# Kernel optimization log

Hardware: AMD Instinct MI355X
Metric: run time of the kernel (lower is better)

## Reference

```python
import jax, jax.numpy as jnp
import numpy as np

B, Q, H, NH, HD = 2, 1024, 2048, 16, 128
QKV_ALPHA = 1e-4   # W8A8B8O8Linear output scale (a)
QKV_BETA = 1.0     # W8A8B8O8Linear bias scale (b)
QK_SCALE = 1e-4    # BMM_S8T_S8N_F32T dequant scale
PV_SCALE = 2e-3    # BMM_S8T_S8N_S8T output scale
DENSE_ALPHA = 1e-5 # W8A8BFP32OFP32Linear dequant scale
INV_NORM = 1.0 / (HD ** 0.5)


def setup_inputs() -> dict:
    key = jax.random.key(0)
    ks = jax.random.split(key, 8)
    hidden_states = jax.random.randint(ks[0], (B, Q, H), -128, 128, dtype=jnp.int32)  # int8 activations
    residual = jax.random.normal(ks[1], (B, Q, H), dtype=jnp.float32)
    alibi = jax.random.normal(ks[2], (B * NH, 1, Q), dtype=jnp.float32) * 0.1
    causal = jnp.triu(jnp.ones((Q, Q), dtype=bool), k=1)  # True = masked (future positions)
    attention_mask = jnp.broadcast_to(causal[None, None], (B, 1, Q, Q))
    w_qkv = jax.random.randint(ks[3], (3 * H, H), -128, 128, dtype=jnp.int32)   # int8 weight
    b_qkv = jax.random.randint(ks[4], (3 * H,), -128, 128, dtype=jnp.int32)     # int8 bias
    w_dense = jax.random.randint(ks[5], (H, H), -128, 128, dtype=jnp.int32)     # int8 weight
    b_dense = jax.random.normal(ks[6], (H,), dtype=jnp.float32)                 # fp32 bias
    return dict(hidden_states=hidden_states, residual=residual, alibi=alibi,
                attention_mask=attention_mask, w_qkv=w_qkv, b_qkv=b_qkv,
                w_dense=w_dense, b_dense=b_dense)


def _quant_i8(x_f32):
    return jnp.clip(jnp.round(x_f32), -128, 127).astype(jnp.int32)


def reference(hidden_states, residual, alibi, attention_mask, w_qkv, b_qkv, w_dense, b_dense):
    # --- W8A8B8O8 fused QKV linear: int8 in, int8 out ---
    acc = jnp.einsum('bqh,oh->bqo', hidden_states, w_qkv)  # exact int32 accumulation
    fused_qkv = _quant_i8(acc.astype(jnp.float32) * QKV_ALPHA + b_qkv.astype(jnp.float32) * QKV_BETA)
    # _split_heads: [B,Q,3H] -> [B,Q,NH,3,HD]
    qkv = fused_qkv.reshape(B, Q, NH, 3, HD)
    q = qkv[..., 0, :].transpose(0, 2, 1, 3).reshape(B * NH, Q, HD)
    k = qkv[..., 1, :].transpose(0, 2, 1, 3).reshape(B * NH, Q, HD)
    v = qkv[..., 2, :].transpose(0, 2, 1, 3).reshape(B * NH, Q, HD)
    # --- BMM_S8T_S8N_F32T: int8 q @ k^T -> fp32 * scale, plus alibi bias ---
    scores_i32 = jnp.einsum('nqd,nkd->nqk', q, k)  # [B*NH,Q,KV] int32
    matmul_result = alibi * 1.0 + scores_i32.astype(jnp.float32) * QK_SCALE * INV_NORM
    attention_scores = matmul_result.reshape(B, NH, Q, Q)
    # masked softmax (True = masked)
    attn_weights = jnp.where(attention_mask, jnp.finfo(jnp.float32).min, attention_scores)
    attention_probs = jax.nn.softmax(attn_weights, axis=-1)
    # quantize probs to int8 with scale 1/127 (BMM_S8T_S8N_S8T A-side)
    p_i8 = _quant_i8(attention_probs * 127.0).reshape(B * NH, Q, Q)
    # --- BMM_S8T_S8N_S8T: int8 probs @ int8 v -> int8 context ---
    ctx_acc = jnp.einsum('nqk,nkd->nqd', p_i8, v)  # int32
    ctx_i8 = _quant_i8(ctx_acc.astype(jnp.float32) * PV_SCALE)
    # _merge_heads: [B*NH,Q,HD] -> [B,Q,H]
    ctx = ctx_i8.reshape(B, NH, Q, HD).transpose(0, 2, 1, 3).reshape(B, Q, H)
    # --- W8A8BFP32OFP32 dense: int8 in, fp32 out ---
    dense_acc = jnp.einsum('bqh,oh->bqo', ctx, w_dense)
    output = dense_acc.astype(jnp.float32) * DENSE_ALPHA + b_dense + residual
    return output
```

## Files before the change

kernel.cpp:

```cpp
#include <hip/hip_runtime.h>
#include <stdint.h>

typedef int i32x4 __attribute__((ext_vector_type(4)));

#define DEV __device__ __forceinline__

DEV void glds16(const void* g, void* l) {
  __builtin_amdgcn_global_load_lds(
      (const __attribute__((address_space(1))) void*)g,
      (__attribute__((address_space(3))) void*)l, 16, 0, 0);
}

DEV int clampi8(float f) {
  int v = (int)rintf(f);
  return v < -128 ? -128 : (v > 127 ? 127 : v);
}

__global__ void pack_all_kernel(const int* __restrict__ s0, const int* __restrict__ s1,
                                const int* __restrict__ s2, int8_t* __restrict__ d0,
                                int8_t* __restrict__ d1, int8_t* __restrict__ d2) {
  const int i = blockIdx.x * 256 + threadIdx.x;
  const int* s;
  int8_t* d;
  int j;
  if (i < 1048576) { s = s0; d = d0; j = i; }
  else if (i < 4194304) { s = s1; d = d1; j = i - 1048576; }
  else { s = s2; d = d2; j = i - 4194304; }
  int4 v = ((const int4*)s)[j];
  char4 c;
  c.x = (char)v.x; c.y = (char)v.y; c.z = (char)v.z; c.w = (char)v.w;
  ((char4*)d)[j] = c;
}

template<int K>
DEV void gemm_core(const int8_t* __restrict__ A, const int8_t* __restrict__ B,
                   int row0, int col0, i32x4 acc[4][4], char* lA, char* lB,
                   int l, int w, int wm, int wn) {
  const int lr = l & 15, lg = l >> 4;
  const int8_t* pA0 = A + (size_t)(row0 + (w * 2 + 0) * 16 + lr) * K + lg * 16;
  const int8_t* pA1 = A + (size_t)(row0 + (w * 2 + 1) * 16 + lr) * K + lg * 16;
  const int8_t* pB0 = B + (size_t)(col0 + (w * 2 + 0) * 16 + lr) * K + lg * 16;
  const int8_t* pB1 = B + (size_t)(col0 + (w * 2 + 1) * 16 + lr) * K + lg * 16;
  glds16(pA0, lA + (w * 2 + 0) * 1024);
  glds16(pA1, lA + (w * 2 + 1) * 1024);
  glds16(pB0, lB + (w * 2 + 0) * 1024);
  glds16(pB1, lB + (w * 2 + 1) * 1024);
  __syncthreads();
  int cur = 0;
  for (int k0 = 0; k0 < K; k0 += 64) {
    const int nxt = cur ^ 1;
    if (k0 + 64 < K) {
      glds16(pA0 + k0 + 64, lA + nxt * 8192 + (w * 2 + 0) * 1024);
      glds16(pA1 + k0 + 64, lA + nxt * 8192 + (w * 2 + 1) * 1024);
      glds16(pB0 + k0 + 64, lB + nxt * 8192 + (w * 2 + 0) * 1024);
      glds16(pB1 + k0 + 64, lB + nxt * 8192 + (w * 2 + 1) * 1024);
    }
    i32x4 a[4], b[4];
#pragma unroll
    for (int i = 0; i < 4; ++i)
      a[i] = *(const i32x4*)(lA + cur * 8192 + ((wm * 4 + i) * 64 + l) * 16);
#pragma unroll
    for (int j = 0; j < 4; ++j)
      b[j] = *(const i32x4*)(lB + cur * 8192 + ((wn * 4 + j) * 64 + l) * 16);
#pragma unroll
    for (int i = 0; i < 4; ++i)
#pragma unroll
      for (int j = 0; j < 4; ++j)
        acc[i][j] = __builtin_amdgcn_mfma_i32_16x16x64_i8(a[i], b[j], acc[i][j], 0, 0, 0);
    __syncthreads();
    cur = nxt;
  }
}

__global__ __launch_bounds__(256) void qkv_kernel(
    const int8_t* __restrict__ hs8, const int8_t* __restrict__ w8,
    const int* __restrict__ bq, int8_t* __restrict__ qb, int8_t* __restrict__ kb,
    int8_t* __restrict__ vT) {
  __shared__ __align__(16) char lA[16384];
  __shared__ __align__(16) char lB[16384];
  const int l = threadIdx.x & 63, w = threadIdx.x >> 6;
  const int wm = w >> 1, wn = w & 1;
  const int lr = l & 15, lg = l >> 4;
  const int row0 = blockIdx.y * 128, col0 = blockIdx.x * 128;
  i32x4 acc[4][4] = {};
  gemm_core<2048>(hs8, w8, row0, col0, acc, lA, lB, l, w, wm, wn);
#pragma unroll
  for (int j = 0; j < 4; ++j) {
    const int col = col0 + (wn * 4 + j) * 16 + lr;
    const float bias = (float)bq[col];
    const int nh = col / 384, rem = col - nh * 384;
    const int s = rem >> 7, d = rem & 127;
#pragma unroll
    for (int i = 0; i < 4; ++i) {
#pragma unroll
      for (int r = 0; r < 4; ++r) {
        const int row = row0 + (wm * 4 + i) * 16 + lg * 4 + r;
        const int bb = row >> 10, qpos = row & 1023;
        const int n = bb * 16 + nh;
        const int8_t c = (int8_t)clampi8((float)acc[i][j][r] * 1e-4f + bias);
        if (s == 0)      qb[((size_t)n << 17) + (qpos << 7) + d] = c;
        else if (s == 1) kb[((size_t)n << 17) + (qpos << 7) + d] = c;
        else             vT[((size_t)n << 17) + (d << 10) + qpos] = c;
      }
    }
  }
}

__global__ __launch_bounds__(256) void attn_stats_kernel(
    const int8_t* __restrict__ qb, const int8_t* __restrict__ kb,
    const float* __restrict__ alibi, float* __restrict__ stats) {
  const int n = blockIdx.y;
  const int tri = blockIdx.x;
  int qt = 0;
  while ((qt + 1) * (qt + 2) / 2 <= tri) ++qt;
  const int kt = tri - qt * (qt + 1) / 2;
  const int l = threadIdx.x & 63, w = threadIdx.x >> 6;
  const int lr = l & 15, lg = l >> 4;
  const int row0 = qt * 128;
  const int8_t* Qh = qb + ((size_t)n << 17);
  const int8_t* Kh = kb + ((size_t)n << 17);
  const float* al = alibi + n * 1024;

  i32x4 qa[2][2];
#pragma unroll
  for (int t = 0; t < 2; ++t)
#pragma unroll
    for (int ks = 0; ks < 2; ++ks)
      qa[t][ks] = *(const i32x4*)(Qh + (size_t)(row0 + (w * 2 + t) * 16 + lr) * 128 + ks * 64 + lg * 16);

  float sf[2][8][4];
#pragma unroll
  for (int nf = 0; nf < 8; ++nf) {
    const size_t krow = (size_t)(kt * 128 + nf * 16 + lr) * 128;
    const i32x4 bk0 = *(const i32x4*)(Kh + krow + lg * 16);
    const i32x4 bk1 = *(const i32x4*)(Kh + krow + 64 + lg * 16);
    const int col = kt * 128 + nf * 16 + lr;
    const float av = al[col];
#pragma unroll
    for (int t = 0; t < 2; ++t) {
      i32x4 sa = {0, 0, 0, 0};
      sa = __builtin_amdgcn_mfma_i32_16x16x64_i8(qa[t][0], bk0, sa, 0, 0, 0);
      sa = __builtin_amdgcn_mfma_i32_16x16x64_i8(qa[t][1], bk1, sa, 0, 0, 0);
#pragma unroll
      for (int r = 0; r < 4; ++r) {
        const int rowg = row0 + (w * 2 + t) * 16 + lg * 4 + r;
        sf[t][nf][r] = (col <= rowg)
            ? av + ((float)sa[r] * 1e-4f) * 0.08838834764831843f
            : -INFINITY;
      }
    }
  }
#pragma unroll
  for (int t = 0; t < 2; ++t)
#pragma unroll
    for (int r = 0; r < 4; ++r) {
      float tm = sf[t][0][r];
#pragma unroll
      for (int nf = 1; nf < 8; ++nf) tm = fmaxf(tm, sf[t][nf][r]);
#pragma unroll
      for (int o = 1; o < 16; o <<= 1) tm = fmaxf(tm, __shfl_xor(tm, o));
      float es = 0.f;
#pragma unroll
      for (int nf = 0; nf < 8; ++nf) es += __expf(sf[t][nf][r] - tm);
#pragma unroll
      for (int o = 1; o < 16; o <<= 1) es += __shfl_xor(es, o);
      if (lr == 0) {
        const int rowl = (w * 2 + t) * 16 + lg * 4 + r;
        float2* st = (float2*)stats;
        st[((n * 8 + qt) * 8 + kt) * 128 + rowl] = make_float2(tm, es);
      }
    }
}

__global__ __launch_bounds__(256) void attn_pv_kernel(
    const int8_t* __restrict__ qb, const int8_t* __restrict__ kb,
    const int8_t* __restrict__ vT, const float* __restrict__ alibi,
    const float* __restrict__ stats, int* __restrict__ slab0,
    int* __restrict__ slab1, int8_t* __restrict__ ctx) {
  __shared__ __align__(16) char lP[128 * 144];
  const int n = blockIdx.y, gi = blockIdx.x;
  int qt, g, kt0, kt1;
  if (gi < 4) { qt = gi; g = 0; kt0 = 0; kt1 = qt + 1; }
  else { const int p = gi - 4; qt = 4 + (p >> 1); g = p & 1; kt0 = g ? 4 : 0; kt1 = g ? qt + 1 : 4; }
  const int l = threadIdx.x & 63, w = threadIdx.x >> 6;
  const int lr = l & 15, lg = l >> 4;
  const int row0 = qt * 128;
  const int8_t* Qh = qb + ((size_t)n << 17);
  const int8_t* Kh = kb + ((size_t)n << 17);
  const int8_t* Vh = vT + ((size_t)n << 17);
  const float* al = alibi + n * 1024;

  i32x4 qa[2][2];
#pragma unroll
  for (int t = 0; t < 2; ++t)
#pragma unroll
    for (int ks = 0; ks < 2; ++ks)
      qa[t][ks] = *(const i32x4*)(Qh + (size_t)(row0 + (w * 2 + t) * 16 + lr) * 128 + ks * 64 + lg * 16);

  float mrow[2][4], srow[2][4];
  const float2* st = (const float2*)stats;
#pragma unroll
  for (int t = 0; t < 2; ++t)
#pragma unroll
    for (int r = 0; r < 4; ++r) {
      const int rowl = (w * 2 + t) * 16 + lg * 4 + r;
      const int base = ((n * 8 + qt) * 8) * 128 + rowl;
      float m = -INFINITY;
      for (int k2 = 0; k2 <= qt; ++k2) m = fmaxf(m, st[base + k2 * 128].x);
      float s = 0.f;
      for (int k2 = 0; k2 <= qt; ++k2) {
        const float2 p = st[base + k2 * 128];
        s += p.y * __expf(p.x - m);
      }
      mrow[t][r] = m; srow[t][r] = s;
    }

  i32x4 pacc[2][8] = {};
  for (int kt = kt0; kt < kt1; ++kt) {
#pragma unroll
    for (int nf = 0; nf < 8; ++nf) {
      const size_t krow = (size_t)(kt * 128 + nf * 16 + lr) * 128;
      const i32x4 bk0 = *(const i32x4*)(Kh + krow + lg * 16);
      const i32x4 bk1 = *(const i32x4*)(Kh + krow + 64 + lg * 16);
      const int col = kt * 128 + nf * 16 + lr;
      const float av = al[col];
#pragma unroll
      for (int t = 0; t < 2; ++t) {
        i32x4 sa = {0, 0, 0, 0};
        sa = __builtin_amdgcn_mfma_i32_16x16x64_i8(qa[t][0], bk0, sa, 0, 0, 0);
        sa = __builtin_amdgcn_mfma_i32_16x16x64_i8(qa[t][1], bk1, sa, 0, 0, 0);
#pragma unroll
        for (int r = 0; r < 4; ++r) {
          const int rowl = (w * 2 + t) * 16 + lg * 4 + r;
          const int rowg = row0 + rowl;
          int p = 0;
          if (col <= rowg) {
            const float s = av + ((float)sa[r] * 1e-4f) * 0.08838834764831843f;
            p = (int)rintf(__expf(s - mrow[t][r]) / srow[t][r] * 127.0f);
          }
          lP[rowl * 144 + nf * 16 + lr] = (char)p;
        }
      }
    }
    __syncthreads();
#pragma unroll
    for (int t = 0; t < 2; ++t) {
      const int rowl = (w * 2 + t) * 16 + lr;
      const i32x4 pa0 = *(const i32x4*)(lP + rowl * 144 + lg * 16);
      const i32x4 pa1 = *(const i32x4*)(lP + rowl * 144 + 64 + lg * 16);
#pragma unroll
      for (int nf = 0; nf < 8; ++nf) {
        const size_t vrow = (size_t)(nf * 16 + lr) * 1024 + kt * 128;
        const i32x4 vb0 = *(const i32x4*)(Vh + vrow + lg * 16);
        const i32x4 vb1 = *(const i32x4*)(Vh + vrow + 64 + lg * 16);
        pacc[t][nf] = __builtin_amdgcn_mfma_i32_16x16x64_i8(pa0, vb0, pacc[t][nf], 0, 0, 0);
        pacc[t][nf] = __builtin_amdgcn_mfma_i32_16x16x64_i8(pa1, vb1, pacc[t][nf], 0, 0, 0);
      }
    }
  }
  const int bb = n >> 4, nh = n & 15;
  if (qt < 4) {
#pragma unroll
    for (int t = 0; t < 2; ++t)
#pragma unroll
      for (int nf = 0; nf < 8; ++nf)
#pragma unroll
        for (int r = 0; r < 4; ++r) {
          const int qpos = row0 + (w * 2 + t) * 16 + lg * 4 + r;
          const int d = nf * 16 + lr;
          ctx[((size_t)(bb * 1024 + qpos)) * 2048 + nh * 128 + d] =
              (int8_t)clampi8((float)pacc[t][nf][r] * 2e-3f);
        }
  } else {
    int* slab = g ? slab1 : slab0;
#pragma unroll
    for (int t = 0; t < 2; ++t)
#pragma unroll
      for (int nf = 0; nf < 8; ++nf)
#pragma unroll
        for (int r = 0; r < 4; ++r) {
          const int qpos = row0 + (w * 2 + t) * 16 + lg * 4 + r;
          const int d = nf * 16 + lr;
          slab[(size_t)(bb * 512 + qpos - 512) * 2048 + nh * 128 + d] = pacc[t][nf][r];
        }
  }
}

__global__ void ctx_reduce_kernel(const int* __restrict__ slab0,
                                  const int* __restrict__ slab1,
                                  int8_t* __restrict__ ctx) {
  const int i = blockIdx.x * blockDim.x + threadIdx.x;
  const int4 a = ((const int4*)slab0)[i];
  const int4 b = ((const int4*)slab1)[i];
  const int elem0 = i * 4;
  const int r512 = elem0 >> 11, col = elem0 & 2047;
  const int bb = r512 >> 9, qpos = 512 + (r512 & 511);
  char4 c;
  c.x = (char)clampi8((float)(a.x + b.x) * 2e-3f);
  c.y = (char)clampi8((float)(a.y + b.y) * 2e-3f);
  c.z = (char)clampi8((float)(a.z + b.z) * 2e-3f);
  c.w = (char)clampi8((float)(a.w + b.w) * 2e-3f);
  ((char4*)ctx)[((size_t)(bb * 1024 + qpos) * 2048 + col) >> 2] = c;
}

__global__ __launch_bounds__(256) void dense_kernel(
    const int8_t* __restrict__ c8, const int8_t* __restrict__ w8,
    const float* __restrict__ bd, const float* __restrict__ res,
    float* __restrict__ out) {
  __shared__ __align__(16) char lA[16384];
  __shared__ __align__(16) char lB[8192];
  const int l = threadIdx.x & 63, w = threadIdx.x >> 6;
  const int wm = w >> 1, wn = w & 1;
  const int lr = l & 15, lg = l >> 4;
  const int row0 = blockIdx.y * 128, col0 = blockIdx.x * 64;
  const int8_t* pA0 = c8 + (size_t)(row0 + (w * 2 + 0) * 16 + lr) * 2048 + lg * 16;
  const int8_t* pA1 = c8 + (size_t)(row0 + (w * 2 + 1) * 16 + lr) * 2048 + lg * 16;
  const int8_t* pB  = w8 + (size_t)(col0 + w * 16 + lr) * 2048 + lg * 16;
  glds16(pA0, lA + (w * 2 + 0) * 1024);
  glds16(pA1, lA + (w * 2 + 1) * 1024);
  glds16(pB,  lB + w * 1024);
  __syncthreads();
  i32x4 acc[4][2] = {};
  int cur = 0;
  for (int k0 = 0; k0 < 2048; k0 += 64) {
    const int nxt = cur ^ 1;
    if (k0 + 64 < 2048) {
      glds16(pA0 + k0 + 64, lA + nxt * 8192 + (w * 2 + 0) * 1024);
      glds16(pA1 + k0 + 64, lA + nxt * 8192 + (w * 2 + 1) * 1024);
      glds16(pB + k0 + 64, lB + nxt * 4096 + w * 1024);
    }
    i32x4 a[4], b[2];
#pragma unroll
    for (int i = 0; i < 4; ++i)
      a[i] = *(const i32x4*)(lA + cur * 8192 + ((wm * 4 + i) * 64 + l) * 16);
#pragma unroll
    for (int j = 0; j < 2; ++j)
      b[j] = *(const i32x4*)(lB + cur * 4096 + ((wn * 2 + j) * 64 + l) * 16);
#pragma unroll
    for (int i = 0; i < 4; ++i)
#pragma unroll
      for (int j = 0; j < 2; ++j)
        acc[i][j] = __builtin_amdgcn_mfma_i32_16x16x64_i8(a[i], b[j], acc[i][j], 0, 0, 0);
    __syncthreads();
    cur = nxt;
  }
#pragma unroll
  for (int j = 0; j < 2; ++j) {
    const int col = col0 + (wn * 2 + j) * 16 + lr;
    const float bias = bd[col];
#pragma unroll
    for (int i = 0; i < 4; ++i) {
#pragma unroll
      for (int r = 0; r < 4; ++r) {
        const int row = row0 + (wm * 4 + i) * 16 + lg * 4 + r;
        const size_t o = (size_t)row * 2048 + col;
        out[o] = (float)acc[i][j][r] * 1e-5f + bias + res[o];
      }
    }
  }
}

extern "C" void kernel_launch(void* const* d_in, const int* in_sizes, int n_in,
                              void* d_out, int out_size, void* d_ws, size_t ws_size,
                              hipStream_t stream) {
  const int* hs = (const int*)d_in[0];
  const float* res = (const float*)d_in[1];
  const float* alibi = (const float*)d_in[2];
  const int* wqkv = (const int*)d_in[4];
  const int* bqkv = (const int*)d_in[5];
  const int* wd = (const int*)d_in[6];
  const float* bd = (const float*)d_in[7];
  float* out = (float*)d_out;
  char* ws = (char*)d_ws;

  int8_t* hs8   = (int8_t*)(ws + 0);
  int8_t* wqkv8 = (int8_t*)(ws + 4194304);
  int*    slab0 = (int*)(ws + 0);
  int*    slab1 = (int*)(ws + 8388608);
  int8_t* wd8   = (int8_t*)(ws + 16777216);
  int8_t* q8b   = (int8_t*)(ws + 20971520);
  int8_t* k8b   = (int8_t*)(ws + 25165824);
  int8_t* vT8   = (int8_t*)(ws + 29360128);
  int8_t* ctx8  = (int8_t*)(ws + 33554432);
  float*  stats = (float*)(ws + 37748736);

  pack_all_kernel<<<20480, 256, 0, stream>>>(hs, wqkv, wd, hs8, wqkv8, wd8);
  qkv_kernel<<<dim3(48, 16), 256, 0, stream>>>(hs8, wqkv8, bqkv, q8b, k8b, vT8);
  attn_stats_kernel<<<dim3(36, 32), 256, 0, stream>>>(q8b, k8b, alibi, stats);
  attn_pv_kernel<<<dim3(12, 32), 256, 0, stream>>>(q8b, k8b, vT8, alibi, stats,
                                                   slab0, slab1, ctx8);
  ctx_reduce_kernel<<<2048, 256, 0, stream>>>(slab0, slab1, ctx8);
  dense_kernel<<<dim3(32, 16), 256, 0, stream>>>(ctx8, wd8, bd, res, out);
}
```

Measured before the change: 197.6 us.

## Split attention PV into two-tile KV chunks with atomic int32 accumulation

The PV kernel now splits every query tile into chunks of at most two KV tiles, which raises the grid from 12 to 20 blocks per head. Partial int32 context sums are combined with atomicAdd into a zeroed full-size accumulator, and a separate kernel then quantizes that accumulator to int8. This replaces the two-slab split plus reduce kernel and aims for better load balance across the causal triangle. In exchange it adds a 16MB zeroing pass, atomic write traffic for every query tile, and a full-size quantize read. A __syncthreads between writing P to LDS and reading it back is also removed, which holds only because each wave reads back just its own rows.

```diff
diff --git a/kernel.cpp b/kernel.cpp
--- a/kernel.cpp
+++ b/kernel.cpp
@@ -30,6 +30,10 @@
   char4 c;
   c.x = (char)v.x; c.y = (char)v.y; c.z = (char)v.z; c.w = (char)v.w;
   ((char4*)d)[j] = c;
+}
+
+__global__ void zero_kernel(int4* __restrict__ p) {
+  p[blockIdx.x * 256 + threadIdx.x] = make_int4(0, 0, 0, 0);
 }
 
 template<int K>
@@ -175,13 +179,13 @@
 __global__ __launch_bounds__(256) void attn_pv_kernel(
     const int8_t* __restrict__ qb, const int8_t* __restrict__ kb,
     const int8_t* __restrict__ vT, const float* __restrict__ alibi,
-    const float* __restrict__ stats, int* __restrict__ slab0,
-    int* __restrict__ slab1, int8_t* __restrict__ ctx) {
+    const float* __restrict__ stats, int* __restrict__ ctxacc) {
   __shared__ __align__(16) char lP[128 * 144];
   const int n = blockIdx.y, gi = blockIdx.x;
-  int qt, g, kt0, kt1;
-  if (gi < 4) { qt = gi; g = 0; kt0 = 0; kt1 = qt + 1; }
-  else { const int p = gi - 4; qt = 4 + (p >> 1); g = p & 1; kt0 = g ? 4 : 0; kt1 = g ? qt + 1 : 4; }
+  int qt = 0, accum = 0;
+  while (accum + ((qt + 2) >> 1) <= gi) { accum += (qt + 2) >> 1; ++qt; }
+  const int c = gi - accum;
+  const int kt0 = 2 * c, kt1 = min(2 * c + 2, qt + 1);
   const int l = threadIdx.x & 63, w = threadIdx.x >> 6;
   const int lr = l & 15, lg = l >> 4;
   const int row0 = qt * 128;
@@ -242,7 +246,6 @@
         }
       }
     }
-    __syncthreads();
 #pragma unroll
     for (int t = 0; t < 2; ++t) {
       const int rowl = (w * 2 + t) * 16 + lr;
@@ -259,48 +262,29 @@
     }
   }
   const int bb = n >> 4, nh = n & 15;
-  if (qt < 4) {
-#pragma unroll
-    for (int t = 0; t < 2; ++t)
-#pragma unroll
-      for (int nf = 0; nf < 8; ++nf)
-#pragma unroll
-        for (int r = 0; r < 4; ++r) {
-          const int qpos = row0 + (w * 2 + t) * 16 + lg * 4 + r;
-          const int d = nf * 16 + lr;
-          ctx[((size_t)(bb * 1024 + qpos)) * 2048 + nh * 128 + d] =
-              (int8_t)clampi8((float)pacc[t][nf][r] * 2e-3f);
-        }
-  } else {
-    int* slab = g ? slab1 : slab0;
-#pragma unroll
-    for (int t = 0; t < 2; ++t)
-#pragma unroll
-      for (int nf = 0; nf < 8; ++nf)
-#pragma unroll
-        for (int r = 0; r < 4; ++r) {
-          const int qpos = row0 + (w * 2 + t) * 16 + lg * 4 + r;
-          const int d = nf * 16 + lr;
-          slab[(size_t)(bb * 512 + qpos - 512) * 2048 + nh * 128 + d] = pacc[t][nf][r];
-        }
-  }
-}
-
-__global__ void ctx_reduce_kernel(const int* __restrict__ slab0,
-                                  const int* __restrict__ slab1,
-                                  int8_t* __restrict__ ctx) {
-  const int i = blockIdx.x * blockDim.x + threadIdx.x;
-  const int4 a = ((const int4*)slab0)[i];
-  const int4 b = ((const int4*)slab1)[i];
-  const int elem0 = i * 4;
-  const int r512 = elem0 >> 11, col = elem0 & 2047;
-  const int bb = r512 >> 9, qpos = 512 + (r512 & 511);
+#pragma unroll
+  for (int t = 0; t < 2; ++t)
+#pragma unroll
+    for (int nf = 0; nf < 8; ++nf)
+#pragma unroll
+      for (int r = 0; r < 4; ++r) {
+        const int qpos = row0 + (w * 2 + t) * 16 + lg * 4 + r;
+        const int d = nf * 16 + lr;
+        atomicAdd(&ctxacc[((size_t)(bb * 1024 + qpos)) * 2048 + nh * 128 + d],
+                  pacc[t][nf][r]);
+      }
+}
+
+__global__ void ctx_quant_kernel(const int* __restrict__ ctxacc,
+                                 int8_t* __restrict__ ctx) {
+  const int i = blockIdx.x * 256 + threadIdx.x;
+  const int4 a = ((const int4*)ctxacc)[i];
   char4 c;
-  c.x = (char)clampi8((float)(a.x + b.x) * 2e-3f);
-  c.y = (char)clampi8((float)(a.y + b.y) * 2e-3f);
-  c.z = (char)clampi8((float)(a.z + b.z) * 2e-3f);
-  c.w = (char)clampi8((float)(a.w + b.w) * 2e-3f);
-  ((char4*)ctx)[((size_t)(bb * 1024 + qpos) * 2048 + col) >> 2] = c;
+  c.x = (char)clampi8((float)a.x * 2e-3f);
+  c.y = (char)clampi8((float)a.y * 2e-3f);
+  c.z = (char)clampi8((float)a.z * 2e-3f);
+  c.w = (char)clampi8((float)a.w * 2e-3f);
+  ((char4*)ctx)[i] = c;
 }
 
 __global__ __launch_bounds__(256) void dense_kernel(
@@ -375,8 +359,7 @@
 
   int8_t* hs8   = (int8_t*)(ws + 0);
   int8_t* wqkv8 = (int8_t*)(ws + 4194304);
-  int*    slab0 = (int*)(ws + 0);
-  int*    slab1 = (int*)(ws + 8388608);
+  int*    ctxacc = (int*)(ws + 0);
   int8_t* wd8   = (int8_t*)(ws + 16777216);
   int8_t* q8b   = (int8_t*)(ws + 20971520);
   int8_t* k8b   = (int8_t*)(ws + 25165824);
@@ -386,9 +369,10 @@
 
   pack_all_kernel<<<20480, 256, 0, stream>>>(hs, wqkv, wd, hs8, wqkv8, wd8);
   qkv_kernel<<<dim3(48, 16), 256, 0, stream>>>(hs8, wqkv8, bqkv, q8b, k8b, vT8);
+  zero_kernel<<<4096, 256, 0, stream>>>((int4*)ctxacc);
   attn_stats_kernel<<<dim3(36, 32), 256, 0, stream>>>(q8b, k8b, alibi, stats);
-  attn_pv_kernel<<<dim3(12, 32), 256, 0, stream>>>(q8b, k8b, vT8, alibi, stats,
-                                                   slab0, slab1, ctx8);
-  ctx_reduce_kernel<<<2048, 256, 0, stream>>>(slab0, slab1, ctx8);
+  attn_pv_kernel<<<dim3(20, 32), 256, 0, stream>>>(q8b, k8b, vT8, alibi, stats,
+                                                   ctxacc);
+  ctx_quant_kernel<<<4096, 256, 0, stream>>>(ctxacc, ctx8);
   dense_kernel<<<dim3(32, 16), 256, 0, stream>>>(ctx8, wd8, bd, res, out);
 }
```

Result: slower. 217.8 us (+10.2%).
